# Optimization experiments

Hardware: AMD Instinct MI355X
Metric: run time of the kernel (lower is better)

Reference implementation:

```python
import jax, jax.numpy as jnp
from jax import lax
import numpy as np

DIM = 8
C = 192
N = 198  # 2 special tokens + 14*14 patches (distilled=True)
B = 1024


def quick_gelu(x):
    return x * jax.nn.sigmoid(1.702 * x)


def setup_inputs() -> dict:
    key = jax.random.key(0)
    ks = jax.random.split(key, 7)
    return {
        "x": jax.random.normal(ks[0], (B, N, C), dtype=jnp.float32),
        "w_down": jax.random.normal(ks[1], (DIM, C), dtype=jnp.float32) * 0.05,
        "b_down": jnp.zeros((DIM,), dtype=jnp.float32),
        "conv_w": jax.random.normal(ks[2], (DIM, DIM, 3, 3), dtype=jnp.float32) * 0.05,
        "conv_b": jnp.zeros((DIM,), dtype=jnp.float32),
        "w_up": jax.random.normal(ks[3], (C, DIM), dtype=jnp.float32) * 0.05,
        "b_up": jnp.zeros((C,), dtype=jnp.float32),
    }


def _conv3x3(t, conv_w, conv_b):
    # t: [B, dim, H, W]; 3x3, stride 1, pad 1 (SAME)
    y = lax.conv_general_dilated(
        t, conv_w, window_strides=(1, 1), padding=((1, 1), (1, 1)),
        dimension_numbers=("NCHW", "OIHW", "NCHW"))
    return y + conv_b[None, :, None, None]


def reference(x, w_down, b_down, conv_w, conv_b, w_up, b_up):
    b, n, c = x.shape
    dim = w_down.shape[0]
    # down projection + QuickGELU
    d = quick_gelu(jnp.einsum("bnc,dc->bnd", x, w_down) + b_down)
    # patch tokens -> [B, dim, 14, 14] -> conv -> [B, 196, dim]
    x_patch = d[:, 2:].reshape(b, 14, 14, dim).transpose(0, 3, 1, 2)
    x_patch = _conv3x3(x_patch, conv_w, conv_b)
    x_patch = x_patch.transpose(0, 2, 3, 1).reshape(b, 14 * 14, dim)
    # cls token -> [B, dim, 1, 1] -> conv (only center tap contributes) -> [B, 1, dim]
    x_cls = d[:, :1].reshape(b, 1, 1, dim).transpose(0, 3, 1, 2)
    x_cls = _conv3x3(x_cls, conv_w, conv_b)
    x_cls = x_cls.transpose(0, 2, 3, 1).reshape(b, 1, dim)
    zero_dist = jnp.zeros_like(x_cls)
    d2 = jnp.concatenate([x_cls, zero_dist, x_patch], axis=1)
    d2 = quick_gelu(d2)  # dropout is identity in eval mode
    return jnp.einsum("bnd,cd->bnc", d2, w_up) + b_up
```

## Files before the change

### kernel.cpp

```cpp
#include <hip/hip_runtime.h>
#include <math.h>

#define NTOK 198
#define CCH  192

typedef float vf4 __attribute__((ext_vector_type(4)));

__device__ __forceinline__ float qgelu(float v) {
    return v / (1.0f + __expf(-1.702f * v));
}

__device__ __forceinline__ float dot8(const float4& a, const float4& wa,
                                      const float4& b, const float4& wb) {
    return a.x*wa.x + a.y*wa.y + a.z*wa.z + a.w*wa.w
         + b.x*wb.x + b.y*wb.y + b.z*wb.z + b.w*wb.w;
}

__global__ __launch_bounds__(256, 2) void convpass_fused(
    const float* __restrict__ x,
    const float* __restrict__ w_down,
    const float* __restrict__ b_down,
    const float* __restrict__ conv_w,
    const float* __restrict__ conv_b,
    const float* __restrict__ w_up,
    const float* __restrict__ b_up,
    float* __restrict__ out)
{
    const int half = blockIdx.x;
    const int b    = blockIdx.y;
    const int tid  = threadIdx.x;

    const int d_start   = half ? 86  : 0;
    const int d_count   = half ? 112 : 114;
    const int out_start = half ? 100 : 0;
    const int out_count = half ? 98  : 100;

    __shared__ float s_w[8 * CCH];
    __shared__ float s_d[114 * 8];
    __shared__ float s_d2[100 * 8];
    __shared__ float s_cw[576];

    for (int t = tid; t < 8 * CCH; t += 256) s_w[t] = w_down[t];
    for (int t = tid; t < 576; t += 256) {
        const int kk = t >> 6, rem = t & 63, o = rem >> 3, i = rem & 7;
        s_cw[t] = conv_w[(o * 8 + i) * 9 + kk];
    }
    __syncthreads();

    {
        const int lane  = tid & 63;
        const int wv    = tid >> 6;
        const int t_sub = lane >> 3;
        const int k     = lane & 7;
        const float bd  = b_down[k];
        const float* xb = x + (size_t)b * NTOK * CCH;

        #pragma unroll 1
        for (int p = 0; p < 2; ++p) {
            const int g  = p * 64 + wv * 16;
            const int iA = g + t_sub;
            const int iB = iA + 8;
            const bool vA = (iA < d_count), vB = (iB < d_count);
            const int nA = d_start + (vA ? iA : 0);
            const int nB = d_start + (vB ? iB : 0);
            const float* pA = xb + (size_t)nA * CCH + k * 24;
            const float* pB = xb + (size_t)nB * CCH + k * 24;

            float accA[8] = {0,0,0,0,0,0,0,0};
            float accB[8] = {0,0,0,0,0,0,0,0};
            #pragma unroll
            for (int h2 = 0; h2 < 2; ++h2) {
                float4 xa[3], xv[3];
                #pragma unroll
                for (int j = 0; j < 3; ++j) {
                    xa[j] = *(const float4*)(pA + h2 * 12 + 4 * j);
                    xv[j] = *(const float4*)(pB + h2 * 12 + 4 * j);
                }
                #pragma unroll
                for (int j = 0; j < 3; ++j) {
                    const int c = k * 24 + h2 * 12 + j * 4;
                    #pragma unroll
                    for (int dm = 0; dm < 8; ++dm) {
                        const float4 wv4 = *(const float4*)&s_w[dm * CCH + c];
                        accA[dm] += xa[j].x*wv4.x + xa[j].y*wv4.y + xa[j].z*wv4.z + xa[j].w*wv4.w;
                        accB[dm] += xv[j].x*wv4.x + xv[j].y*wv4.y + xv[j].z*wv4.z + xv[j].w*wv4.w;
                    }
                }
            }
            float oA = 0.f, oB = 0.f;
            #pragma unroll
            for (int dm = 0; dm < 8; ++dm) {
                float a = accA[dm];
                a += __shfl_xor(a, 1); a += __shfl_xor(a, 2); a += __shfl_xor(a, 4);
                float c = accB[dm];
                c += __shfl_xor(c, 1); c += __shfl_xor(c, 2); c += __shfl_xor(c, 4);
                oA = (dm == k) ? a : oA;
                oB = (dm == k) ? c : oB;
            }
            if (vA) s_d[iA * 8 + k] = qgelu(oA + bd);
            if (vB) s_d[iB * 8 + k] = qgelu(oB + bd);
        }
    }
    __syncthreads();

    for (int j = tid; j < out_count * 8; j += 256) {
        const int nr = j >> 3, o = j & 7;
        const int n = out_start + nr;
        if (n == 1) {
            s_d2[j] = 0.0f;
        } else if (n == 0) {
            const float4 d0 = *(const float4*)&s_d[0];
            const float4 d1 = *(const float4*)&s_d[4];
            const float4 w0 = *(const float4*)&s_cw[4 * 64 + o * 8];
            const float4 w1 = *(const float4*)&s_cw[4 * 64 + o * 8 + 4];
            s_d2[j] = qgelu(conv_b[o] + dot8(d0, w0, d1, w1));
        } else {
            const int pos = n - 2, h = pos / 14, w = pos % 14;
            float acc = conv_b[o];
            #pragma unroll
            for (int dh = -1; dh <= 1; ++dh) {
                const int hh = h + dh;
                if (hh < 0 || hh > 13) continue;
                #pragma unroll
                for (int dw = -1; dw <= 1; ++dw) {
                    const int ww = w + dw;
                    if (ww < 0 || ww > 13) continue;
                    const int tok = 2 + hh * 14 + ww;
                    const int kk  = (dh + 1) * 3 + (dw + 1);
                    const int ti  = tok - d_start;
                    const float4 d0 = *(const float4*)&s_d[ti * 8];
                    const float4 d1 = *(const float4*)&s_d[ti * 8 + 4];
                    const float4 w0 = *(const float4*)&s_cw[kk * 64 + o * 8];
                    const float4 w1 = *(const float4*)&s_cw[kk * 64 + o * 8 + 4];
                    acc += dot8(d0, w0, d1, w1);
                }
            }
            s_d2[j] = qgelu(acc);
        }
    }
    __syncthreads();

    const int c4 = tid % 48;
    const int tl = tid / 48;
    if (tl < 5) {
        float w_r[4][8];
        #pragma unroll
        for (int cc = 0; cc < 4; ++cc) {
            const float4 wa = *(const float4*)(w_up + (c4 * 4 + cc) * 8);
            const float4 wb = *(const float4*)(w_up + (c4 * 4 + cc) * 8 + 4);
            w_r[cc][0] = wa.x; w_r[cc][1] = wa.y; w_r[cc][2] = wa.z; w_r[cc][3] = wa.w;
            w_r[cc][4] = wb.x; w_r[cc][5] = wb.y; w_r[cc][6] = wb.z; w_r[cc][7] = wb.w;
        }
        const float4 bu = *(const float4*)(b_up + c4 * 4);
        float* outb = out + ((size_t)b * NTOK + out_start) * CCH;
        #pragma unroll 1
        for (int nr = tl; nr < out_count; nr += 5) {
            const float4 da = *(const float4*)&s_d2[nr * 8];
            const float4 dv = *(const float4*)&s_d2[nr * 8 + 4];
            float accs[4] = {bu.x, bu.y, bu.z, bu.w};
            #pragma unroll
            for (int cc = 0; cc < 4; ++cc) {
                accs[cc] += da.x * w_r[cc][0] + da.y * w_r[cc][1]
                          + da.z * w_r[cc][2] + da.w * w_r[cc][3]
                          + dv.x * w_r[cc][4] + dv.y * w_r[cc][5]
                          + dv.z * w_r[cc][6] + dv.w * w_r[cc][7];
            }
            const vf4 r = {accs[0], accs[1], accs[2], accs[3]};
            __builtin_nontemporal_store(r, (vf4*)(outb + (size_t)nr * CCH + c4 * 4));
        }
    }
}

extern "C" void kernel_launch(void* const* d_in, const int* in_sizes, int n_in,
                              void* d_out, int out_size, void* d_ws, size_t ws_size,
                              hipStream_t stream) {
    const float* x      = (const float*)d_in[0];
    const float* w_down = (const float*)d_in[1];
    const float* b_down = (const float*)d_in[2];
    const float* conv_w = (const float*)d_in[3];
    const float* conv_b = (const float*)d_in[4];
    const float* w_up   = (const float*)d_in[5];
    const float* b_up   = (const float*)d_in[6];
    float* out = (float*)d_out;

    const int B = in_sizes[0] / (NTOK * CCH);
    convpass_fused<<<dim3(2, B), dim3(256), 0, stream>>>(
        x, w_down, b_down, conv_w, conv_b, w_up, b_up, out);
}
```

Baseline: 82.92 us.

## Raise occupancy by cutting register use in down and up projection loops

Launch bounds go from 2 to 4 blocks per CU, and both GEMM-like phases are reshaped to hold fewer live registers. The down projection now loads 8-wide x chunks across 3 iterations instead of 12-wide across 2. The up projection switches from 240 threads writing 4 channels each to 192 threads writing 2 channels each, using float2 nontemporal stores. The aim is more resident waves to hide latency on this memory-bound kernel, at the cost of narrower stores and fewer active threads in the output phase.

```diff
diff --git a/kernel.cpp b/kernel.cpp
--- a/kernel.cpp
+++ b/kernel.cpp
@@ -4,6 +4,7 @@
 #define NTOK 198
 #define CCH  192
 
+typedef float vf2 __attribute__((ext_vector_type(2)));
 typedef float vf4 __attribute__((ext_vector_type(4)));
 
 __device__ __forceinline__ float qgelu(float v) {
@@ -16,7 +17,7 @@
          + b.x*wb.x + b.y*wb.y + b.z*wb.z + b.w*wb.w;
 }
 
-__global__ __launch_bounds__(256, 2) void convpass_fused(
+__global__ __launch_bounds__(256, 4) void convpass_fused(
     const float* __restrict__ x,
     const float* __restrict__ w_down,
     const float* __restrict__ b_down,
@@ -57,8 +58,7 @@
 
         #pragma unroll 1
         for (int p = 0; p < 2; ++p) {
-            const int g  = p * 64 + wv * 16;
-            const int iA = g + t_sub;
+            const int iA = p * 64 + wv * 16 + t_sub;
             const int iB = iA + 8;
             const bool vA = (iA < d_count), vB = (iB < d_count);
             const int nA = d_start + (vA ? iA : 0);
@@ -69,22 +69,17 @@
             float accA[8] = {0,0,0,0,0,0,0,0};
             float accB[8] = {0,0,0,0,0,0,0,0};
             #pragma unroll
-            for (int h2 = 0; h2 < 2; ++h2) {
-                float4 xa[3], xv[3];
+            for (int h3 = 0; h3 < 3; ++h3) {
+                const float4 xa0 = *(const float4*)(pA + h3 * 8);
+                const float4 xa1 = *(const float4*)(pA + h3 * 8 + 4);
+                const float4 xv0 = *(const float4*)(pB + h3 * 8);
+                const float4 xv1 = *(const float4*)(pB + h3 * 8 + 4);
                 #pragma unroll
-                for (int j = 0; j < 3; ++j) {
-                    xa[j] = *(const float4*)(pA + h2 * 12 + 4 * j);
-                    xv[j] = *(const float4*)(pB + h2 * 12 + 4 * j);
-                }
-                #pragma unroll
-                for (int j = 0; j < 3; ++j) {
-                    const int c = k * 24 + h2 * 12 + j * 4;
-                    #pragma unroll
-                    for (int dm = 0; dm < 8; ++dm) {
-                        const float4 wv4 = *(const float4*)&s_w[dm * CCH + c];
-                        accA[dm] += xa[j].x*wv4.x + xa[j].y*wv4.y + xa[j].z*wv4.z + xa[j].w*wv4.w;
-                        accB[dm] += xv[j].x*wv4.x + xv[j].y*wv4.y + xv[j].z*wv4.z + xv[j].w*wv4.w;
-                    }
+                for (int dm = 0; dm < 8; ++dm) {
+                    const float4 w0 = *(const float4*)&s_w[dm * CCH + k * 24 + h3 * 8];
+                    const float4 w1 = *(const float4*)&s_w[dm * CCH + k * 24 + h3 * 8 + 4];
+                    accA[dm] += dot8(xa0, w0, xa1, w1);
+                    accB[dm] += dot8(xv0, w0, xv1, w1);
                 }
             }
             float oA = 0.f, oB = 0.f;
@@ -140,33 +135,23 @@
     }
     __syncthreads();
 
-    const int c4 = tid % 48;
-    const int tl = tid / 48;
-    if (tl < 5) {
-        float w_r[4][8];
-        #pragma unroll
-        for (int cc = 0; cc < 4; ++cc) {
-            const float4 wa = *(const float4*)(w_up + (c4 * 4 + cc) * 8);
-            const float4 wb = *(const float4*)(w_up + (c4 * 4 + cc) * 8 + 4);
-            w_r[cc][0] = wa.x; w_r[cc][1] = wa.y; w_r[cc][2] = wa.z; w_r[cc][3] = wa.w;
-            w_r[cc][4] = wb.x; w_r[cc][5] = wb.y; w_r[cc][6] = wb.z; w_r[cc][7] = wb.w;
-        }
-        const float4 bu = *(const float4*)(b_up + c4 * 4);
+    const int c2 = tid % 96;
+    const int tl = tid / 96;
+    if (tl < 2) {
+        const int ch = c2 * 2;
+        const float4 wa0 = *(const float4*)(w_up + ch * 8);
+        const float4 wa1 = *(const float4*)(w_up + ch * 8 + 4);
+        const float4 wb0 = *(const float4*)(w_up + ch * 8 + 8);
+        const float4 wb1 = *(const float4*)(w_up + ch * 8 + 12);
+        const float bu0 = b_up[ch], bu1 = b_up[ch + 1];
         float* outb = out + ((size_t)b * NTOK + out_start) * CCH;
         #pragma unroll 1
-        for (int nr = tl; nr < out_count; nr += 5) {
+        for (int nr = tl; nr < out_count; nr += 2) {
             const float4 da = *(const float4*)&s_d2[nr * 8];
             const float4 dv = *(const float4*)&s_d2[nr * 8 + 4];
-            float accs[4] = {bu.x, bu.y, bu.z, bu.w};
-            #pragma unroll
-            for (int cc = 0; cc < 4; ++cc) {
-                accs[cc] += da.x * w_r[cc][0] + da.y * w_r[cc][1]
-                          + da.z * w_r[cc][2] + da.w * w_r[cc][3]
-                          + dv.x * w_r[cc][4] + dv.y * w_r[cc][5]
-                          + dv.z * w_r[cc][6] + dv.w * w_r[cc][7];
-            }
-            const vf4 r = {accs[0], accs[1], accs[2], accs[3]};
-            __builtin_nontemporal_store(r, (vf4*)(outb + (size_t)nr * CCH + c4 * 4));
+            const vf2 r = {bu0 + dot8(da, wa0, dv, wa1),
+                           bu1 + dot8(da, wb0, dv, wb1)};
+            __builtin_nontemporal_store(r, (vf2*)(outb + (size_t)nr * CCH + ch));
         }
     }
 }
```

Measured after the change: 220.8 us. 2.66x slower.

## Keep down-projection weights in registers and reduce one token per wave

Applied to the files above, without the earlier changes.

Removes the shared-memory copy of w_down. Each lane now holds 24 weights for one (dim, channel-chunk) pair in registers, and each wave processes one token per iteration, reducing across chunks with cross-lane shuffles. The launch-bounds occupancy target rises from 2 to 4 blocks, and conv_b is staged in shared memory. The cost is more serial loop iterations, each a single token with shuffle reductions, and the 8 dim lanes issue redundant broadcast x loads.

```diff
diff --git a/kernel.cpp b/kernel.cpp
--- a/kernel.cpp
+++ b/kernel.cpp
@@ -16,7 +16,7 @@
          + b.x*wb.x + b.y*wb.y + b.z*wb.z + b.w*wb.w;
 }
 
-__global__ __launch_bounds__(256, 2) void convpass_fused(
+__global__ __launch_bounds__(256, 4) void convpass_fused(
     const float* __restrict__ x,
     const float* __restrict__ w_down,
     const float* __restrict__ b_down,
@@ -35,70 +35,51 @@
     const int out_start = half ? 100 : 0;
     const int out_count = half ? 98  : 100;
 
-    __shared__ float s_w[8 * CCH];
     __shared__ float s_d[114 * 8];
     __shared__ float s_d2[100 * 8];
     __shared__ float s_cw[576];
+    __shared__ float s_cb[8];
 
-    for (int t = tid; t < 8 * CCH; t += 256) s_w[t] = w_down[t];
     for (int t = tid; t < 576; t += 256) {
         const int kk = t >> 6, rem = t & 63, o = rem >> 3, i = rem & 7;
         s_cw[t] = conv_w[(o * 8 + i) * 9 + kk];
     }
-    __syncthreads();
+    if (tid < 8) s_cb[tid] = conv_b[tid];
 
     {
         const int lane  = tid & 63;
         const int wv    = tid >> 6;
-        const int t_sub = lane >> 3;
-        const int k     = lane & 7;
-        const float bd  = b_down[k];
-        const float* xb = x + (size_t)b * NTOK * CCH;
+        const int chunk = lane >> 3;
+        const int dim   = lane & 7;
+
+        float wreg[24];
+        {
+            const float* wp = w_down + dim * CCH + chunk * 24;
+            #pragma unroll
+            for (int j = 0; j < 24; ++j) wreg[j] = wp[j];
+        }
+        const float bd  = b_down[dim];
+        const float* xb = x + (size_t)b * NTOK * CCH + chunk * 24;
 
         #pragma unroll 1
-        for (int p = 0; p < 2; ++p) {
-            const int g  = p * 64 + wv * 16;
-            const int iA = g + t_sub;
-            const int iB = iA + 8;
-            const bool vA = (iA < d_count), vB = (iB < d_count);
-            const int nA = d_start + (vA ? iA : 0);
-            const int nB = d_start + (vB ? iB : 0);
-            const float* pA = xb + (size_t)nA * CCH + k * 24;
-            const float* pB = xb + (size_t)nB * CCH + k * 24;
-
-            float accA[8] = {0,0,0,0,0,0,0,0};
-            float accB[8] = {0,0,0,0,0,0,0,0};
+        for (int i = 0; i < 29; ++i) {
+            const int idx = i * 4 + wv;
+            const bool valid = (idx < d_count);
+            const int n = d_start + (valid ? idx : 0);
+            const float* xr = xb + (size_t)n * CCH;
+            float a0 = 0.f, a1 = 0.f;
             #pragma unroll
-            for (int h2 = 0; h2 < 2; ++h2) {
-                float4 xa[3], xv[3];
-                #pragma unroll
-                for (int j = 0; j < 3; ++j) {
-                    xa[j] = *(const float4*)(pA + h2 * 12 + 4 * j);
-                    xv[j] = *(const float4*)(pB + h2 * 12 + 4 * j);
-                }
-                #pragma unroll
-                for (int j = 0; j < 3; ++j) {
-                    const int c = k * 24 + h2 * 12 + j * 4;
-                    #pragma unroll
-                    for (int dm = 0; dm < 8; ++dm) {
-                        const float4 wv4 = *(const float4*)&s_w[dm * CCH + c];
-                        accA[dm] += xa[j].x*wv4.x + xa[j].y*wv4.y + xa[j].z*wv4.z + xa[j].w*wv4.w;
-                        accB[dm] += xv[j].x*wv4.x + xv[j].y*wv4.y + xv[j].z*wv4.z + xv[j].w*wv4.w;
-                    }
-                }
+            for (int j = 0; j < 3; ++j) {
+                const float4 xv = *(const float4*)(xr + j * 8);
+                const float4 xw = *(const float4*)(xr + j * 8 + 4);
+                a0 += xv.x*wreg[j*8]   + xv.y*wreg[j*8+1] + xv.z*wreg[j*8+2] + xv.w*wreg[j*8+3];
+                a1 += xw.x*wreg[j*8+4] + xw.y*wreg[j*8+5] + xw.z*wreg[j*8+6] + xw.w*wreg[j*8+7];
             }
-            float oA = 0.f, oB = 0.f;
-            #pragma unroll
-            for (int dm = 0; dm < 8; ++dm) {
-                float a = accA[dm];
-                a += __shfl_xor(a, 1); a += __shfl_xor(a, 2); a += __shfl_xor(a, 4);
-                float c = accB[dm];
-                c += __shfl_xor(c, 1); c += __shfl_xor(c, 2); c += __shfl_xor(c, 4);
-                oA = (dm == k) ? a : oA;
-                oB = (dm == k) ? c : oB;
-            }
-            if (vA) s_d[iA * 8 + k] = qgelu(oA + bd);
-            if (vB) s_d[iB * 8 + k] = qgelu(oB + bd);
+            float acc = a0 + a1;
+            acc += __shfl_xor(acc, 8);
+            acc += __shfl_xor(acc, 16);
+            acc += __shfl_xor(acc, 32);
+            if (valid && lane < 8) s_d[idx * 8 + dim] = qgelu(acc + bd);
         }
     }
     __syncthreads();
@@ -113,10 +94,10 @@
             const float4 d1 = *(const float4*)&s_d[4];
             const float4 w0 = *(const float4*)&s_cw[4 * 64 + o * 8];
             const float4 w1 = *(const float4*)&s_cw[4 * 64 + o * 8 + 4];
-            s_d2[j] = qgelu(conv_b[o] + dot8(d0, w0, d1, w1));
+            s_d2[j] = qgelu(s_cb[o] + dot8(d0, w0, d1, w1));
         } else {
             const int pos = n - 2, h = pos / 14, w = pos % 14;
-            float acc = conv_b[o];
+            float acc = s_cb[o];
             #pragma unroll
             for (int dh = -1; dh <= 1; ++dh) {
                 const int hh = h + dh;
```

Result: faster. 77.67 us (-6.3%).
